# Kernel optimization log

Measured on AMD Instinct MI355X. Metric: run time of the kernel, lower is better.

## Reference

```python
import jax, jax.numpy as jnp
import numpy as np

H, W, C, B = 16, 16, 2048, 32
HEADS = 4
D1, D2 = 256, 128


def _build_edges(h, w):
    """Lattice + mirror + disease-node + self-loop edges (PyG GATConv default adds self loops)."""
    idx = lambda i, j: i * w + j
    edges = []
    for i in range(h):
        for j in range(w):
            if i + 1 < h:
                edges += [(idx(i, j), idx(i + 1, j)), (idx(i + 1, j), idx(i, j))]
            if j + 1 < w:
                edges += [(idx(i, j), idx(i, j + 1)), (idx(i, j + 1), idx(i, j))]
            mj = w - j - 1
            if mj != j:
                edges.append((idx(i, j), idx(i, mj)))
    n = h * w
    for i in range(n):  # disease node (index n), bidirectional
        edges += [(i, n), (n, i)]
    for i in range(n + 1):  # self loops
        edges.append((i, i))
    e = np.asarray(edges, dtype=np.int32)
    return jnp.asarray(e[:, 0]), jnp.asarray(e[:, 1])


def setup_inputs() -> dict:
    key = jax.random.key(0)
    ks = jax.random.split(key, 16)
    s = 0.02
    src, dst = _build_edges(H, W)
    return {
        "fmap": jax.random.normal(ks[0], (B, C, H, W), jnp.float32),
        "W1": jax.random.normal(ks[1], (C, HEADS * D1), jnp.float32) * s,
        "a_src1": jax.random.normal(ks[2], (HEADS, D1), jnp.float32) * s,
        "a_dst1": jax.random.normal(ks[3], (HEADS, D1), jnp.float32) * s,
        "b1": jnp.zeros((D1,), jnp.float32),
        "W2": jax.random.normal(ks[4], (D1, HEADS * D2), jnp.float32) * s,
        "a_src2": jax.random.normal(ks[5], (HEADS, D2), jnp.float32) * s,
        "a_dst2": jax.random.normal(ks[6], (HEADS, D2), jnp.float32) * s,
        "b2": jnp.zeros((D2,), jnp.float32),
        "Wp": jax.random.normal(ks[7], (D2, 1), jnp.float32) * s,
        "bp": jnp.zeros((1,), jnp.float32),
        "Wc1": jax.random.normal(ks[8], (D2, 64), jnp.float32) * s,
        "bc1": jnp.zeros((64,), jnp.float32),
        "Wc2": jax.random.normal(ks[9], (64, 1), jnp.float32) * s,
        "bc2": jnp.zeros((1,), jnp.float32),
        "src": src,
        "dst": dst,
    }


def _gat_layer(x, src, dst, Wm, a_s, a_d, b, heads, out_dim):
    """PyG GATConv math: concat=False (mean over heads), leaky_relu slope 0.2."""
    N = x.shape[0]
    h = (x @ Wm).reshape(N, heads, out_dim)           # [N, H, D]
    es = jnp.sum(h * a_s, axis=-1)                    # [N, H]
    ed = jnp.sum(h * a_d, axis=-1)                    # [N, H]
    e = jax.nn.leaky_relu(es[src] + ed[dst], 0.2)     # [E, H]
    m = jax.ops.segment_max(e, dst, num_segments=N)   # softmax over incoming edges
    alpha = jnp.exp(e - m[dst])
    denom = jax.ops.segment_sum(alpha, dst, num_segments=N)
    alpha = alpha / (denom[dst] + 1e-16)
    agg = jax.ops.segment_sum(alpha[:, :, None] * h[src], dst, num_segments=N)
    return agg.mean(axis=1) + b                       # [N, D]


def reference(fmap, W1, a_src1, a_dst1, b1, W2, a_src2, a_dst2, b2,
              Wp, bp, Wc1, bc1, Wc2, bc2, src, dst):
    Bn, Cc, Hh, Ww = fmap.shape
    nodes = fmap.reshape(Bn, Cc, Hh * Ww).transpose(0, 2, 1)   # [B, HW, C]
    nodes = jnp.concatenate([nodes, jnp.zeros((Bn, 1, Cc), nodes.dtype)], axis=1)

    def per_graph(x):
        x = _gat_layer(x, src, dst, W1, a_src1, a_dst1, b1, HEADS, D1)
        x = _gat_layer(x, src, dst, W2, a_src2, a_dst2, b2, HEADS, D2)
        w = jax.nn.sigmoid(x @ Wp + bp)               # [N, 1] attention pool weights
        g = jnp.mean(x * w, axis=0)                   # global_mean_pool, single graph
        h1 = jax.nn.relu(g @ Wc1 + bc1)
        pred = jax.nn.sigmoid(h1 @ Wc2 + bc2)         # [1]
        return pred[0], w[:, 0]

    preds, atts = jax.vmap(per_graph)(nodes)          # [B], [B, N]
    return preds, atts
```

## Files before the change

### kernel.cpp

```cpp
#include <hip/hip_runtime.h>

typedef __bf16 bf16_t;
typedef __bf16 bf16x8 __attribute__((ext_vector_type(8)));
typedef float f32x4 __attribute__((ext_vector_type(4)));

#define MPAD  8320
#define NNODE 257
#define NB    32

__device__ __forceinline__ void gld_lds16(const bf16_t* g, bf16_t* l) {
    __builtin_amdgcn_global_load_lds(
        (const __attribute__((address_space(1))) void*)g,
        (__attribute__((address_space(3))) void*)l, 16, 0, 0);
}

__global__ __launch_bounds__(256) void prep_x_kernel(const float* __restrict__ fmap,
                                                     bf16_t* __restrict__ X) {
    __shared__ float tile[64][65];
    int c0 = blockIdx.x * 64, n0 = blockIdx.y * 64, b = blockIdx.z;
    int t = threadIdx.x;
    const float* f = fmap + (size_t)b * 2048 * 256;
    int ln = t & 63, lc = t >> 6;
#pragma unroll
    for (int i = 0; i < 16; i++) {
        int c = lc + i * 4;
        tile[c][ln] = f[(size_t)(c0 + c) * 256 + n0 + ln];
    }
    __syncthreads();
    int sn = t >> 3, sc = (t & 7) * 8;
#pragma unroll
    for (int half = 0; half < 2; half++) {
        int n = sn + half * 32;
        bf16_t tmp[8];
#pragma unroll
        for (int j = 0; j < 8; j++) tmp[j] = (bf16_t)tile[sc + j][n];
        *(bf16x8*)&X[(size_t)(b * 257 + n0 + n) * 2048 + c0 + sc] = *(bf16x8*)tmp;
    }
}

__global__ __launch_bounds__(256) void prep_w_kernel(const float* __restrict__ W,
                                                     bf16_t* __restrict__ Wt,
                                                     int K, int N) {
    __shared__ float tile[32][33];
    int k0 = blockIdx.x * 32, n0 = blockIdx.y * 32;
    int tx = threadIdx.x, ty = threadIdx.y;
#pragma unroll
    for (int i = 0; i < 4; i++)
        tile[ty + i * 8][tx] = W[(size_t)(k0 + ty + i * 8) * N + n0 + tx];
    __syncthreads();
#pragma unroll
    for (int i = 0; i < 4; i++)
        Wt[(size_t)(n0 + ty + i * 8) * K + k0 + tx] = (bf16_t)tile[tx][ty + i * 8];
}

__global__ void build_csr_kernel(const int* __restrict__ dstv, int E,
                                 int* __restrict__ indptr, int* __restrict__ eidx) {
    __shared__ int cnt[258];
    __shared__ int off[258];
    int t = threadIdx.x;
    for (int i = t; i < 258; i += 256) cnt[i] = 0;
    __syncthreads();
    for (int e = t; e < E; e += 256) atomicAdd(&cnt[dstv[e] + 1], 1);
    __syncthreads();
    if (t == 0) {
        int s = 0;
        for (int i = 0; i < 258; i++) { s += cnt[i]; off[i] = s; }
    }
    __syncthreads();
    for (int i = t; i < 258; i += 256) indptr[i] = off[i];
    __syncthreads();
    for (int e = t; e < E; e += 256) {
        int p = atomicAdd(&off[dstv[e]], 1);
        eidx[p] = e;
    }
}

__global__ __launch_bounds__(256) void gemm_kernel(const bf16_t* __restrict__ A,
                                                   const bf16_t* __restrict__ Bt,
                                                   bf16_t* __restrict__ C,
                                                   int K, int N) {
    __shared__ __align__(16) bf16_t sm[3 * 8192];
    int row0 = blockIdx.y * 128, col0 = blockIdx.x * 128;
    int t = threadIdx.x;
    int wave = t >> 6, lane = t & 63;
    int wr = wave >> 1, wc = wave & 1;
    int ch0 = wave * 2;
    int srow = lane >> 2;
    int scol = (lane & 3) * 8;
    const bf16_t* Abase = A + (size_t)row0 * K;
    const bf16_t* Bbase = Bt + (size_t)col0 * K;
    f32x4 acc[4][4] = {};
    int fr = lane & 15;
    int kq = (lane >> 4) * 8;
    int nk = K >> 5;
    auto issue = [&](int kt, int stage) {
        bf16_t* As = sm + stage * 8192;
        bf16_t* Bs = As + 4096;
        int k0 = kt << 5;
#pragma unroll
        for (int c = 0; c < 2; c++) {
            int chunk = ch0 + c;
            int row = chunk * 16 + srow;
            gld_lds16(Abase + (size_t)row * K + k0 + scol, &As[chunk * 512]);
            gld_lds16(Bbase + (size_t)row * K + k0 + scol, &Bs[chunk * 512]);
        }
    };
    issue(0, 0);
    if (nk > 1) issue(1, 1);
    for (int k = 0; k < nk; k++) {
        int cur = k % 3;
        if (k + 2 < nk) {
            issue(k + 2, (k + 2) % 3);
            asm volatile("s_waitcnt vmcnt(8)" ::: "memory");
        } else if (k + 1 < nk) {
            asm volatile("s_waitcnt vmcnt(4)" ::: "memory");
        } else {
            asm volatile("s_waitcnt vmcnt(0)" ::: "memory");
        }
        __builtin_amdgcn_s_barrier();
        const bf16_t* As = sm + cur * 8192;
        const bf16_t* Bs = As + 4096;
        bf16x8 af[4], bfv[4];
#pragma unroll
        for (int mr = 0; mr < 4; mr++)
            af[mr] = *(const bf16x8*)&As[(wr * 64 + mr * 16 + fr) * 32 + kq];
#pragma unroll
        for (int nc = 0; nc < 4; nc++)
            bfv[nc] = *(const bf16x8*)&Bs[(wc * 64 + nc * 16 + fr) * 32 + kq];
#pragma unroll
        for (int mr = 0; mr < 4; mr++)
#pragma unroll
            for (int nc = 0; nc < 4; nc++)
                acc[mr][nc] = __builtin_amdgcn_mfma_f32_16x16x32_bf16(
                    af[mr], bfv[nc], acc[mr][nc], 0, 0, 0);
        asm volatile("s_waitcnt lgkmcnt(0)" ::: "memory");
        __builtin_amdgcn_s_barrier();
    }
#pragma unroll
    for (int mr = 0; mr < 4; mr++) {
        int crow = row0 + wr * 64 + mr * 16 + (lane >> 4) * 4;
#pragma unroll
        for (int nc = 0; nc < 4; nc++) {
            int ccol = col0 + wc * 64 + nc * 16 + (lane & 15);
#pragma unroll
            for (int r = 0; r < 4; r++)
                C[(size_t)(crow + r) * N + ccol] = (bf16_t)acc[mr][nc][r];
        }
    }
}

template<int D>
__global__ __launch_bounds__(256) void esed_kernel(const bf16_t* __restrict__ Hb,
                                                   const float* __restrict__ a_s,
                                                   const float* __restrict__ a_d,
                                                   float* __restrict__ es,
                                                   float* __restrict__ ed) {
    constexpr int VPL = D / 64;
    int r = blockIdx.x;
    int h = threadIdx.x >> 6, lane = threadIdx.x & 63;
    const bf16_t* row = Hb + (size_t)r * 4 * D + h * D + lane * VPL;
    const float* asp = a_s + h * D + lane * VPL;
    const float* adp = a_d + h * D + lane * VPL;
    bf16_t xv[VPL];
    __builtin_memcpy(xv, row, VPL * 2);
    float ss = 0.f, sd = 0.f;
#pragma unroll
    for (int v = 0; v < VPL; v++) {
        float x = (float)xv[v];
        ss += x * asp[v];
        sd += x * adp[v];
    }
#pragma unroll
    for (int o = 32; o > 0; o >>= 1) {
        ss += __shfl_down(ss, o);
        sd += __shfl_down(sd, o);
    }
    if (lane == 0) { es[r * 4 + h] = ss; ed[r * 4 + h] = sd; }
}

template<int D>
__global__ __launch_bounds__(256) void attn_kernel(const bf16_t* __restrict__ Hb,
                                                   const float* __restrict__ es,
                                                   const float* __restrict__ ed,
                                                   const int* __restrict__ indptr,
                                                   const int* __restrict__ eidx,
                                                   const int* __restrict__ srcv,
                                                   const float* __restrict__ bias,
                                                   float* __restrict__ outf,
                                                   bf16_t* __restrict__ outb) {
    constexpr int VPL = D / 64;
    int d = blockIdx.x, b = blockIdx.y;
    int r = b * 257 + d;
    int t = threadIdx.x, wv = t >> 6, lane = t & 63;
    int e0 = indptr[d];
    int deg = indptr[d + 1] - e0;
    __shared__ float alpha[NNODE * 4];
    __shared__ int   ssh[NNODE];
    __shared__ float wred[4][8];
    __shared__ float mh4[4], rh4[4];
    __shared__ float osh[4][D];
    const float4 edv = *(const float4*)&ed[r * 4];
    float edh[4] = {edv.x, edv.y, edv.z, edv.w};
    float lmax[4] = {-1e30f, -1e30f, -1e30f, -1e30f};
    for (int i = t; i < deg; i += 256) {
        int s = srcv[eidx[e0 + i]];
        ssh[i] = s;
        float4 e4 = *(const float4*)&es[(b * 257 + s) * 4];
        float ev[4] = {e4.x, e4.y, e4.z, e4.w};
#pragma unroll
        for (int h = 0; h < 4; h++) {
            float v = ev[h] + edh[h];
            v = v > 0.f ? v : 0.2f * v;
            alpha[i * 4 + h] = v;
            lmax[h] = fmaxf(lmax[h], v);
        }
    }
#pragma unroll
    for (int h = 0; h < 4; h++) {
        float m = lmax[h];
#pragma unroll
        for (int o = 32; o > 0; o >>= 1) m = fmaxf(m, __shfl_down(m, o));
        if (lane == 0) wred[h][wv] = m;
    }
    __syncthreads();
    if (t < 4)
        mh4[t] = fmaxf(fmaxf(wred[t][0], wred[t][1]), fmaxf(wred[t][2], wred[t][3]));
    __syncthreads();
    float lsum[4] = {0.f, 0.f, 0.f, 0.f};
    for (int i = t; i < deg; i += 256) {
#pragma unroll
        for (int h = 0; h < 4; h++) {
            float a = __expf(alpha[i * 4 + h] - mh4[h]);
            alpha[i * 4 + h] = a;
            lsum[h] += a;
        }
    }
#pragma unroll
    for (int h = 0; h < 4; h++) {
        float s = lsum[h];
#pragma unroll
        for (int o = 32; o > 0; o >>= 1) s += __shfl_down(s, o);
        if (lane == 0) wred[h][wv] = s;
    }
    __syncthreads();
    if (t < 4)
        rh4[t] = 1.f / (wred[t][0] + wred[t][1] + wred[t][2] + wred[t][3] + 1e-16f);
    __syncthreads();
    for (int i = t; i < deg; i += 256) {
#pragma unroll
        for (int h = 0; h < 4; h++) alpha[i * 4 + h] *= rh4[h];
    }
    __syncthreads();
    float acc[VPL] = {};
    const bf16_t* hb = Hb + (size_t)(b * 257) * 4 * D + wv * D + lane * VPL;
    for (int i = 0; i < deg; i++) {
        float a = alpha[i * 4 + wv];
        const bf16_t* hr = hb + (size_t)ssh[i] * 4 * D;
        bf16_t xv[VPL];
        __builtin_memcpy(xv, hr, VPL * 2);
#pragma unroll
        for (int v = 0; v < VPL; v++) acc[v] += a * (float)xv[v];
    }
#pragma unroll
    for (int v = 0; v < VPL; v++) osh[wv][lane * VPL + v] = acc[v];
    __syncthreads();
    if (t < D) {
        float o = (osh[0][t] + osh[1][t] + osh[2][t] + osh[3][t]) * 0.25f + bias[t];
        if (outb) outb[(size_t)r * D + t] = (bf16_t)o;
        else      outf[(size_t)r * D + t] = o;
    }
}

__global__ __launch_bounds__(256) void head_kernel(const float* __restrict__ out2,
                                                   const float* __restrict__ Wp,
                                                   const float* __restrict__ bp,
                                                   const float* __restrict__ Wc1,
                                                   const float* __restrict__ bc1,
                                                   const float* __restrict__ Wc2,
                                                   const float* __restrict__ bc2,
                                                   float* __restrict__ outp) {
    int b = blockIdx.x, t = threadIdx.x, wv = t >> 6, lane = t & 63;
    __shared__ float wsh[NNODE];
    __shared__ float gpart[2][128];
    __shared__ float gsh[128];
    __shared__ float h1[64];
    const float* X = out2 + (size_t)b * 257 * 128;
    float wp0 = Wp[lane], wp1 = Wp[64 + lane], bp0 = bp[0];
    for (int n = wv; n < 257; n += 4) {
        const float* xr = X + n * 128;
        float s = xr[lane] * wp0 + xr[64 + lane] * wp1;
#pragma unroll
        for (int o = 32; o > 0; o >>= 1) s += __shfl_down(s, o);
        if (lane == 0) {
            float wvv = 1.f / (1.f + __expf(-(s + bp0)));
            wsh[n] = wvv;
            outp[32 + b * 257 + n] = wvv;
        }
    }
    __syncthreads();
    {
        int dim = t & 127, half = t >> 7;
        float s = 0.f;
        for (int n = half; n < 257; n += 2) s += X[n * 128 + dim] * wsh[n];
        gpart[half][dim] = s;
    }
    __syncthreads();
    if (t < 128) gsh[t] = (gpart[0][t] + gpart[1][t]) * (1.f / 257.f);
    __syncthreads();
    if (t < 64) {
        float s = bc1[t];
        for (int k = 0; k < 128; k++) s += gsh[k] * Wc1[k * 64 + t];
        h1[t] = fmaxf(s, 0.f);
    }
    __syncthreads();
    if (t == 0) {
        float s = bc2[0];
        for (int j = 0; j < 64; j++) s += h1[j] * Wc2[j];
        outp[b] = 1.f / (1.f + expf(-s));
    }
}

extern "C" void kernel_launch(void* const* d_in, const int* in_sizes, int n_in,
                              void* d_out, int out_size, void* d_ws, size_t ws_size,
                              hipStream_t stream) {
    const float* fmap   = (const float*)d_in[0];
    const float* W1     = (const float*)d_in[1];
    const float* a_src1 = (const float*)d_in[2];
    const float* a_dst1 = (const float*)d_in[3];
    const float* b1     = (const float*)d_in[4];
    const float* W2     = (const float*)d_in[5];
    const float* a_src2 = (const float*)d_in[6];
    const float* a_dst2 = (const float*)d_in[7];
    const float* b2     = (const float*)d_in[8];
    const float* Wp     = (const float*)d_in[9];
    const float* bp     = (const float*)d_in[10];
    const float* Wc1    = (const float*)d_in[11];
    const float* bc1    = (const float*)d_in[12];
    const float* Wc2    = (const float*)d_in[13];
    const float* bc2    = (const float*)d_in[14];
    const int*   srcv   = (const int*)d_in[15];
    const int*   dstv   = (const int*)d_in[16];
    int E = in_sizes[15];
    float* outp = (float*)d_out;

    char* w = (char*)d_ws;
    size_t off = 0;
    auto alloc = [&](size_t bytes) -> void* {
        void* p = w + off;
        off += (bytes + 255) & ~(size_t)255;
        return p;
    };
    bf16_t* X    = (bf16_t*)alloc((size_t)MPAD * 2048 * sizeof(bf16_t));
    bf16_t* W1t  = (bf16_t*)alloc((size_t)1024 * 2048 * sizeof(bf16_t));
    bf16_t* W2t  = (bf16_t*)alloc((size_t)512 * 256 * sizeof(bf16_t));
    bf16_t* H1   = (bf16_t*)alloc((size_t)MPAD * 1024 * sizeof(bf16_t));
    float*  es1  = (float*)alloc((size_t)MPAD * 4 * sizeof(float));
    float*  ed1  = (float*)alloc((size_t)MPAD * 4 * sizeof(float));
    bf16_t* out1 = (bf16_t*)alloc((size_t)MPAD * 256 * sizeof(bf16_t));
    bf16_t* H2   = (bf16_t*)alloc((size_t)MPAD * 512 * sizeof(bf16_t));
    float*  es2  = (float*)alloc((size_t)MPAD * 4 * sizeof(float));
    float*  ed2  = (float*)alloc((size_t)MPAD * 4 * sizeof(float));
    float*  out2 = (float*)alloc((size_t)MPAD * 128 * sizeof(float));
    int*  indptr = (int*)alloc(258 * sizeof(int));
    int*  eidx   = (int*)alloc((size_t)E * sizeof(int));

    hipMemsetAsync(X, 0, (size_t)MPAD * 2048 * sizeof(bf16_t), stream);
    hipMemsetAsync(out1 + (size_t)8224 * 256, 0,
                   (size_t)(MPAD - 8224) * 256 * sizeof(bf16_t), stream);

    prep_w_kernel<<<dim3(64, 32), dim3(32, 8), 0, stream>>>(W1, W1t, 2048, 1024);
    prep_w_kernel<<<dim3(8, 16), dim3(32, 8), 0, stream>>>(W2, W2t, 256, 512);
    prep_x_kernel<<<dim3(32, 4, NB), 256, 0, stream>>>(fmap, X);
    build_csr_kernel<<<1, 256, 0, stream>>>(dstv, E, indptr, eidx);

    gemm_kernel<<<dim3(1024 / 128, MPAD / 128), 256, 0, stream>>>(X, W1t, H1, 2048, 1024);
    esed_kernel<256><<<NB * NNODE, 256, 0, stream>>>(H1, a_src1, a_dst1, es1, ed1);
    attn_kernel<256><<<dim3(NNODE, NB), 256, 0, stream>>>(H1, es1, ed1, indptr, eidx,
                                                          srcv, b1, nullptr, out1);
    gemm_kernel<<<dim3(512 / 128, MPAD / 128), 256, 0, stream>>>(out1, W2t, H2, 256, 512);
    esed_kernel<128><<<NB * NNODE, 256, 0, stream>>>(H2, a_src2, a_dst2, es2, ed2);
    attn_kernel<128><<<dim3(NNODE, NB), 256, 0, stream>>>(H2, es2, ed2, indptr, eidx,
                                                          srcv, b2, out2, nullptr);
    head_kernel<<<NB, 256, 0, stream>>>(out2, Wp, bp, Wc1, bc1, Wc2, bc2, outp);

    (void)n_in; (void)out_size; (void)ws_size;
}
```

Before: 374.8 us.

## Merge setup kernels, fuse attention-logit dots into GEMM epilogue, retile GEMM

Folds the weight transposes, fmap transpose, buffer zeroing and CSR build into one setup kernel, replacing two full memsets with targeted zeroing of only the pad rows. The per-row es/ed dot products now run in the GEMM epilogue and are accumulated with atomics, which removes the separate esed kernels and their reread of H. The GEMM moves to 128 threads per block, with each wave computing a 64x128 sub-tile and twice the accumulators. The attention kernel applies the softmax normalisation inline, dropping one LDS pass and a barrier. The trade-offs are fewer waves per GEMM tile with more register pressure, plus atomic contention on es/ed.

```diff
diff --git a/kernel.cpp b/kernel.cpp
--- a/kernel.cpp
+++ b/kernel.cpp
@@ -14,82 +14,99 @@
         (__attribute__((address_space(3))) void*)l, 16, 0, 0);
 }
 
-__global__ __launch_bounds__(256) void prep_x_kernel(const float* __restrict__ fmap,
-                                                     bf16_t* __restrict__ X) {
-    __shared__ float tile[64][65];
-    int c0 = blockIdx.x * 64, n0 = blockIdx.y * 64, b = blockIdx.z;
-    int t = threadIdx.x;
-    const float* f = fmap + (size_t)b * 2048 * 256;
-    int ln = t & 63, lc = t >> 6;
-#pragma unroll
-    for (int i = 0; i < 16; i++) {
-        int c = lc + i * 4;
-        tile[c][ln] = f[(size_t)(c0 + c) * 256 + n0 + ln];
-    }
-    __syncthreads();
-    int sn = t >> 3, sc = (t & 7) * 8;
-#pragma unroll
-    for (int half = 0; half < 2; half++) {
-        int n = sn + half * 32;
-        bf16_t tmp[8];
-#pragma unroll
-        for (int j = 0; j < 8; j++) tmp[j] = (bf16_t)tile[sc + j][n];
-        *(bf16x8*)&X[(size_t)(b * 257 + n0 + n) * 2048 + c0 + sc] = *(bf16x8*)tmp;
-    }
-}
-
-__global__ __launch_bounds__(256) void prep_w_kernel(const float* __restrict__ W,
-                                                     bf16_t* __restrict__ Wt,
-                                                     int K, int N) {
-    __shared__ float tile[32][33];
-    int k0 = blockIdx.x * 32, n0 = blockIdx.y * 32;
-    int tx = threadIdx.x, ty = threadIdx.y;
-#pragma unroll
-    for (int i = 0; i < 4; i++)
-        tile[ty + i * 8][tx] = W[(size_t)(k0 + ty + i * 8) * N + n0 + tx];
-    __syncthreads();
-#pragma unroll
-    for (int i = 0; i < 4; i++)
-        Wt[(size_t)(n0 + ty + i * 8) * K + k0 + tx] = (bf16_t)tile[tx][ty + i * 8];
-}
-
-__global__ void build_csr_kernel(const int* __restrict__ dstv, int E,
-                                 int* __restrict__ indptr, int* __restrict__ eidx) {
-    __shared__ int cnt[258];
-    __shared__ int off[258];
-    int t = threadIdx.x;
-    for (int i = t; i < 258; i += 256) cnt[i] = 0;
-    __syncthreads();
-    for (int e = t; e < E; e += 256) atomicAdd(&cnt[dstv[e] + 1], 1);
-    __syncthreads();
-    if (t == 0) {
-        int s = 0;
-        for (int i = 0; i < 258; i++) { s += cnt[i]; off[i] = s; }
-    }
-    __syncthreads();
-    for (int i = t; i < 258; i += 256) indptr[i] = off[i];
-    __syncthreads();
-    for (int e = t; e < E; e += 256) {
-        int p = atomicAdd(&off[dstv[e]], 1);
-        eidx[p] = e;
-    }
-}
-
-__global__ __launch_bounds__(256) void gemm_kernel(const bf16_t* __restrict__ A,
-                                                   const bf16_t* __restrict__ Bt,
-                                                   bf16_t* __restrict__ C,
-                                                   int K, int N) {
+__global__ __launch_bounds__(256) void setup_kernel(const float* __restrict__ W1, bf16_t* __restrict__ W1t,
+                                                    const float* __restrict__ W2, bf16_t* __restrict__ W2t,
+                                                    const float* __restrict__ fmap, bf16_t* __restrict__ X,
+                                                    const int* __restrict__ dstv, int E,
+                                                    int* __restrict__ indptr, int* __restrict__ eidx,
+                                                    float* __restrict__ zbase, bf16_t* __restrict__ out1) {
+    __shared__ float smem[64 * 65];
+    int idx = blockIdx.x, t = threadIdx.x;
+    if (idx < 2176) {
+        const float* W; bf16_t* Wt; int K, N, kt, nt;
+        if (idx < 2048) { W = W1; Wt = W1t; K = 2048; N = 1024; kt = idx >> 5; nt = idx & 31; }
+        else { int l = idx - 2048; W = W2; Wt = W2t; K = 256; N = 512; kt = l >> 4; nt = l & 15; }
+        int k0 = kt * 32, n0 = nt * 32;
+        int tx = t & 31, ty = t >> 5;
+#pragma unroll
+        for (int i = 0; i < 4; i++)
+            smem[(ty + i * 8) * 33 + tx] = W[(size_t)(k0 + ty + i * 8) * N + n0 + tx];
+        __syncthreads();
+#pragma unroll
+        for (int i = 0; i < 4; i++)
+            Wt[(size_t)(n0 + ty + i * 8) * K + k0 + tx] = (bf16_t)smem[tx * 33 + ty + i * 8];
+    } else if (idx < 6272) {
+        int local = idx - 2176;
+        int ct = local & 31, rem = local >> 5;
+        int nt = rem & 3, b = rem >> 2;
+        int c0 = ct * 64, n0 = nt * 64;
+        const float* f = fmap + (size_t)b * 2048 * 256;
+        int ln = t & 63, lc = t >> 6;
+#pragma unroll
+        for (int i = 0; i < 16; i++) {
+            int c = lc + i * 4;
+            smem[c * 65 + ln] = f[(size_t)(c0 + c) * 256 + n0 + ln];
+        }
+        __syncthreads();
+        int sn = t >> 3, sc = (t & 7) * 8;
+#pragma unroll
+        for (int half = 0; half < 2; half++) {
+            int n = sn + half * 32;
+            bf16_t tmp[8];
+#pragma unroll
+            for (int j = 0; j < 8; j++) tmp[j] = (bf16_t)smem[(sc + j) * 65 + n];
+            *(bf16x8*)&X[(size_t)(b * 257 + n0 + n) * 2048 + c0 + sc] = *(bf16x8*)tmp;
+        }
+    } else if (idx < 6402) {
+        int local = idx - 6272;
+        uint4* p = (uint4*)zbase + (size_t)local * 256;
+        p[t] = uint4{0, 0, 0, 0};
+    } else if (idx < 6530) {
+        int i = idx - 6402;
+        int row = (i < 32) ? (i * 257 + 256) : (8224 + (i - 32));
+        uint4* p = (uint4*)(X + (size_t)row * 2048);
+        p[t] = uint4{0, 0, 0, 0};
+    } else if (idx < 6542) {
+        int local = idx - 6530;
+        uint4* p = (uint4*)((char*)(out1 + (size_t)8224 * 256) + (size_t)local * 4096);
+        p[t] = uint4{0, 0, 0, 0};
+    } else {
+        __shared__ int cnt[258];
+        __shared__ int off[258];
+        for (int i = t; i < 258; i += 256) cnt[i] = 0;
+        __syncthreads();
+        for (int e = t; e < E; e += 256) atomicAdd(&cnt[dstv[e] + 1], 1);
+        __syncthreads();
+        if (t == 0) {
+            int s = 0;
+            for (int i = 0; i < 258; i++) { s += cnt[i]; off[i] = s; }
+        }
+        __syncthreads();
+        for (int i = t; i < 258; i += 256) indptr[i] = off[i];
+        __syncthreads();
+        for (int e = t; e < E; e += 256) {
+            int p = atomicAdd(&off[dstv[e]], 1);
+            eidx[p] = e;
+        }
+    }
+}
+
+__global__ __launch_bounds__(128, 2) void gemm_kernel(const bf16_t* __restrict__ A,
+                                                      const bf16_t* __restrict__ Bt,
+                                                      bf16_t* __restrict__ C,
+                                                      const float* __restrict__ asrc,
+                                                      const float* __restrict__ adst,
+                                                      float* __restrict__ es,
+                                                      float* __restrict__ ed,
+                                                      int K, int N, int headD) {
     __shared__ __align__(16) bf16_t sm[3 * 8192];
     int row0 = blockIdx.y * 128, col0 = blockIdx.x * 128;
     int t = threadIdx.x;
     int wave = t >> 6, lane = t & 63;
-    int wr = wave >> 1, wc = wave & 1;
-    int ch0 = wave * 2;
-    int srow = lane >> 2;
-    int scol = (lane & 3) * 8;
+    int srow = lane >> 2, scol = (lane & 3) * 8;
     const bf16_t* Abase = A + (size_t)row0 * K;
     const bf16_t* Bbase = Bt + (size_t)col0 * K;
-    f32x4 acc[4][4] = {};
+    f32x4 acc[4][8] = {};
     int fr = lane & 15;
     int kq = (lane >> 4) * 8;
     int nk = K >> 5;
@@ -98,8 +115,8 @@
         bf16_t* Bs = As + 4096;
         int k0 = kt << 5;
 #pragma unroll
-        for (int c = 0; c < 2; c++) {
-            int chunk = ch0 + c;
+        for (int c = 0; c < 4; c++) {
+            int chunk = wave * 4 + c;
             int row = chunk * 16 + srow;
             gld_lds16(Abase + (size_t)row * K + k0 + scol, &As[chunk * 512]);
             gld_lds16(Bbase + (size_t)row * K + k0 + scol, &Bs[chunk * 512]);
@@ -111,26 +128,26 @@
         int cur = k % 3;
         if (k + 2 < nk) {
             issue(k + 2, (k + 2) % 3);
+            asm volatile("s_waitcnt vmcnt(16)" ::: "memory");
+        } else if (k + 1 < nk) {
             asm volatile("s_waitcnt vmcnt(8)" ::: "memory");
-        } else if (k + 1 < nk) {
-            asm volatile("s_waitcnt vmcnt(4)" ::: "memory");
         } else {
             asm volatile("s_waitcnt vmcnt(0)" ::: "memory");
         }
         __builtin_amdgcn_s_barrier();
         const bf16_t* As = sm + cur * 8192;
         const bf16_t* Bs = As + 4096;
-        bf16x8 af[4], bfv[4];
+        bf16x8 af[4], bfv[8];
 #pragma unroll
         for (int mr = 0; mr < 4; mr++)
-            af[mr] = *(const bf16x8*)&As[(wr * 64 + mr * 16 + fr) * 32 + kq];
-#pragma unroll
-        for (int nc = 0; nc < 4; nc++)
-            bfv[nc] = *(const bf16x8*)&Bs[(wc * 64 + nc * 16 + fr) * 32 + kq];
+            af[mr] = *(const bf16x8*)&As[(wave * 64 + mr * 16 + fr) * 32 + kq];
+#pragma unroll
+        for (int nc = 0; nc < 8; nc++)
+            bfv[nc] = *(const bf16x8*)&Bs[(nc * 16 + fr) * 32 + kq];
 #pragma unroll
         for (int mr = 0; mr < 4; mr++)
 #pragma unroll
-            for (int nc = 0; nc < 4; nc++)
+            for (int nc = 0; nc < 8; nc++)
                 acc[mr][nc] = __builtin_amdgcn_mfma_f32_16x16x32_bf16(
                     af[mr], bfv[nc], acc[mr][nc], 0, 0, 0);
         asm volatile("s_waitcnt lgkmcnt(0)" ::: "memory");
@@ -138,44 +155,45 @@
     }
 #pragma unroll
     for (int mr = 0; mr < 4; mr++) {
-        int crow = row0 + wr * 64 + mr * 16 + (lane >> 4) * 4;
-#pragma unroll
-        for (int nc = 0; nc < 4; nc++) {
-            int ccol = col0 + wc * 64 + nc * 16 + (lane & 15);
+        int crow = row0 + wave * 64 + mr * 16 + (lane >> 4) * 4;
+#pragma unroll
+        for (int nc = 0; nc < 8; nc++) {
+            int ccol = col0 + nc * 16 + (lane & 15);
 #pragma unroll
             for (int r = 0; r < 4; r++)
                 C[(size_t)(crow + r) * N + ccol] = (bf16_t)acc[mr][nc][r];
         }
     }
-}
-
-template<int D>
-__global__ __launch_bounds__(256) void esed_kernel(const bf16_t* __restrict__ Hb,
-                                                   const float* __restrict__ a_s,
-                                                   const float* __restrict__ a_d,
-                                                   float* __restrict__ es,
-                                                   float* __restrict__ ed) {
-    constexpr int VPL = D / 64;
-    int r = blockIdx.x;
-    int h = threadIdx.x >> 6, lane = threadIdx.x & 63;
-    const bf16_t* row = Hb + (size_t)r * 4 * D + h * D + lane * VPL;
-    const float* asp = a_s + h * D + lane * VPL;
-    const float* adp = a_d + h * D + lane * VPL;
-    bf16_t xv[VPL];
-    __builtin_memcpy(xv, row, VPL * 2);
-    float ss = 0.f, sd = 0.f;
-#pragma unroll
-    for (int v = 0; v < VPL; v++) {
-        float x = (float)xv[v];
-        ss += x * asp[v];
-        sd += x * adp[v];
-    }
-#pragma unroll
-    for (int o = 32; o > 0; o >>= 1) {
-        ss += __shfl_down(ss, o);
-        sd += __shfl_down(sd, o);
-    }
-    if (lane == 0) { es[r * 4 + h] = ss; ed[r * 4 + h] = sd; }
+    int h = col0 / headD;
+    float as_v[8], ad_v[8];
+#pragma unroll
+    for (int nc = 0; nc < 8; nc++) {
+        int ccol = col0 + nc * 16 + (lane & 15);
+        as_v[nc] = asrc[ccol];
+        ad_v[nc] = adst[ccol];
+    }
+#pragma unroll
+    for (int mr = 0; mr < 4; mr++)
+#pragma unroll
+        for (int r = 0; r < 4; r++) {
+            float ps = 0.f, pd = 0.f;
+#pragma unroll
+            for (int nc = 0; nc < 8; nc++) {
+                float v = acc[mr][nc][r];
+                ps += v * as_v[nc];
+                pd += v * ad_v[nc];
+            }
+#pragma unroll
+            for (int m = 1; m < 16; m <<= 1) {
+                ps += __shfl_xor(ps, m);
+                pd += __shfl_xor(pd, m);
+            }
+            if ((lane & 15) == 0) {
+                int row = row0 + wave * 64 + mr * 16 + (lane >> 4) * 4 + r;
+                atomicAdd(&es[row * 4 + h], ps);
+                atomicAdd(&ed[row * 4 + h], pd);
+            }
+        }
 }
 
 template<int D>
@@ -246,15 +264,11 @@
     if (t < 4)
         rh4[t] = 1.f / (wred[t][0] + wred[t][1] + wred[t][2] + wred[t][3] + 1e-16f);
     __syncthreads();
-    for (int i = t; i < deg; i += 256) {
-#pragma unroll
-        for (int h = 0; h < 4; h++) alpha[i * 4 + h] *= rh4[h];
-    }
-    __syncthreads();
+    float rh = rh4[wv];
     float acc[VPL] = {};
     const bf16_t* hb = Hb + (size_t)(b * 257) * 4 * D + wv * D + lane * VPL;
     for (int i = 0; i < deg; i++) {
-        float a = alpha[i * 4 + wv];
+        float a = alpha[i * 4 + wv] * rh;
         const bf16_t* hr = hb + (size_t)ssh[i] * 4 * D;
         bf16_t xv[VPL];
         __builtin_memcpy(xv, hr, VPL * 2);
@@ -354,31 +368,24 @@
     bf16_t* W1t  = (bf16_t*)alloc((size_t)1024 * 2048 * sizeof(bf16_t));
     bf16_t* W2t  = (bf16_t*)alloc((size_t)512 * 256 * sizeof(bf16_t));
     bf16_t* H1   = (bf16_t*)alloc((size_t)MPAD * 1024 * sizeof(bf16_t));
+    bf16_t* out1 = (bf16_t*)alloc((size_t)MPAD * 256 * sizeof(bf16_t));
+    bf16_t* H2   = (bf16_t*)alloc((size_t)MPAD * 512 * sizeof(bf16_t));
+    float*  out2 = (float*)alloc((size_t)MPAD * 128 * sizeof(float));
     float*  es1  = (float*)alloc((size_t)MPAD * 4 * sizeof(float));
     float*  ed1  = (float*)alloc((size_t)MPAD * 4 * sizeof(float));
-    bf16_t* out1 = (bf16_t*)alloc((size_t)MPAD * 256 * sizeof(bf16_t));
-    bf16_t* H2   = (bf16_t*)alloc((size_t)MPAD * 512 * sizeof(bf16_t));
     float*  es2  = (float*)alloc((size_t)MPAD * 4 * sizeof(float));
     float*  ed2  = (float*)alloc((size_t)MPAD * 4 * sizeof(float));
-    float*  out2 = (float*)alloc((size_t)MPAD * 128 * sizeof(float));
     int*  indptr = (int*)alloc(258 * sizeof(int));
     int*  eidx   = (int*)alloc((size_t)E * sizeof(int));
 
-    hipMemsetAsync(X, 0, (size_t)MPAD * 2048 * sizeof(bf16_t), stream);
-    hipMemsetAsync(out1 + (size_t)8224 * 256, 0,
-                   (size_t)(MPAD - 8224) * 256 * sizeof(bf16_t), stream);
-
-    prep_w_kernel<<<dim3(64, 32), dim3(32, 8), 0, stream>>>(W1, W1t, 2048, 1024);
-    prep_w_kernel<<<dim3(8, 16), dim3(32, 8), 0, stream>>>(W2, W2t, 256, 512);
-    prep_x_kernel<<<dim3(32, 4, NB), 256, 0, stream>>>(fmap, X);
-    build_csr_kernel<<<1, 256, 0, stream>>>(dstv, E, indptr, eidx);
-
-    gemm_kernel<<<dim3(1024 / 128, MPAD / 128), 256, 0, stream>>>(X, W1t, H1, 2048, 1024);
-    esed_kernel<256><<<NB * NNODE, 256, 0, stream>>>(H1, a_src1, a_dst1, es1, ed1);
+    setup_kernel<<<6543, 256, 0, stream>>>(W1, W1t, W2, W2t, fmap, X, dstv, E,
+                                           indptr, eidx, es1, out1);
+    gemm_kernel<<<dim3(1024 / 128, MPAD / 128), 128, 0, stream>>>(
+        X, W1t, H1, a_src1, a_dst1, es1, ed1, 2048, 1024, 256);
     attn_kernel<256><<<dim3(NNODE, NB), 256, 0, stream>>>(H1, es1, ed1, indptr, eidx,
                                                           srcv, b1, nullptr, out1);
-    gemm_kernel<<<dim3(512 / 128, MPAD / 128), 256, 0, stream>>>(out1, W2t, H2, 256, 512);
-    esed_kernel<128><<<NB * NNODE, 256, 0, stream>>>(H2, a_src2, a_dst2, es2, ed2);
+    gemm_kernel<<<dim3(512 / 128, MPAD / 128), 128, 0, stream>>>(
+        out1, W2t, H2, a_src2, a_dst2, es2, ed2, 256, 512, 128);
     attn_kernel<128><<<dim3(NNODE, NB), 256, 0, stream>>>(H2, es2, ed2, indptr, eidx,
                                                           srcv, b2, out2, nullptr);
     head_kernel<<<NB, 256, 0, stream>>>(out2, Wp, bp, Wc1, bc1, Wc2, bc2, outp);
```

Measured after the change: 355.0 us. 5.3% less time.
